# Kernel optimization log

Measured on AMD Instinct MI355X. Metric: run time of the kernel, lower is better.

The kernel has to match this reference:

```python
import jax, jax.numpy as jnp
import numpy as np

N, D_IN, D_ATTN = 8192, 48, 8


def setup_inputs() -> dict:
    key = jax.random.key(0)
    ks = jax.random.split(key, 9)
    s = 1.0 / np.sqrt(D_IN)
    return {
        "x": jax.random.normal(ks[0], (N, D_IN), jnp.float32),
        "Kw": jax.random.normal(ks[1], (D_IN, D_ATTN), jnp.float32) * s,
        "Kb": jax.random.normal(ks[2], (D_ATTN,), jnp.float32) * s,
        "Qw": jax.random.normal(ks[3], (D_IN, D_ATTN), jnp.float32) * s,
        "Qb": jax.random.normal(ks[4], (D_ATTN,), jnp.float32) * s,
        "Vw": jax.random.normal(ks[5], (D_IN, D_ATTN), jnp.float32) * s,
        "Vb": jax.random.normal(ks[6], (D_ATTN,), jnp.float32) * s,
        "Zw": jax.random.normal(ks[7], (D_ATTN, D_IN), jnp.float32) * (1.0 / np.sqrt(D_ATTN)),
        "Zb": jax.random.normal(ks[8], (D_IN,), jnp.float32) * (1.0 / np.sqrt(D_ATTN)),
    }


def reference(x, Kw, Kb, Qw, Qb, Vw, Vb, Zw, Zb):
    # Tiny QKV projections: [N,48] -> [N,8]
    Xk = x @ Kw + Kb
    Xq = x @ Qw + Qb
    Xv = x @ Vw + Vb
    # Attention over the batch/row dimension: [N,8]@[8,N] -> [N,N]
    scale = jnp.sqrt(jnp.asarray(D_ATTN, jnp.float32))
    AM = jax.nn.softmax(Xk @ Xq.T / scale, axis=1)  # torch F.softmax 2D default dim=1
    Z = AM @ Xv                                      # [N,8]
    return x + (Z @ Zw + Zb)                         # residual + output proj [N,48]
```

## Files before the change

### kernel.cpp

```cpp
#include <hip/hip_runtime.h>
#include <hip/hip_fp16.h>


#define QV_OFF   32768
#define BMAX_OFF 98304
#define PART_OFF 98560

typedef _Float16 hv2 __attribute__((ext_vector_type(2)));
union HVU { unsigned u; hv2 v; };

static __device__ __forceinline__ unsigned pku(float a, float b) {
    auto t = __builtin_amdgcn_cvt_pkrtz(a, b);
    union { decltype(t) x; unsigned u; } c; c.x = t; return c.u;
}
static __device__ __forceinline__ hv2 asV(unsigned u) { HVU t; t.u = u; return t.v; }
static __device__ __forceinline__ hv2 h2fma(hv2 a, hv2 b, hv2 c) {
#if __has_builtin(__builtin_elementwise_fma)
    return __builtin_elementwise_fma(a, b, c);
#else
    union { hv2 v; __half2 h; } A, B, C, D;
    A.v = a; B.v = b; C.v = c;
    D.h = __hfma2(A.h, B.h, C.h);
    return D.v;
#endif
}
static __device__ __forceinline__ unsigned dupL(unsigned u) {
    const unsigned lo = u & 0xFFFFu; return lo | (lo << 16);
}
static __device__ __forceinline__ unsigned dupH(unsigned u) {
    const unsigned hi = u >> 16; return hi | (hi << 16);
}

__global__ __launch_bounds__(256) void proj_kernel(
    const float* __restrict__ x,
    const float* __restrict__ Kw, const float* __restrict__ Kb,
    const float* __restrict__ Qw, const float* __restrict__ Qb,
    const float* __restrict__ Vw, const float* __restrict__ Vb,
    unsigned* __restrict__ Xksf16, unsigned* __restrict__ QV,
    float* __restrict__ bmax)
{
    __shared__ float xs[32 * 49];
    __shared__ float wAll[3 * 388];
    __shared__ float bs[24];
    __shared__ float outv[32][25];
    const int tid = threadIdx.x;
    const int r0 = blockIdx.x * 32;

    for (int i = tid; i < 1536; i += 256) {
        int r = i / 48, c = i - r * 48;
        xs[r * 49 + c] = x[r0 * 48 + i];
    }
    for (int i = tid; i < 384; i += 256) {
        wAll[i]       = Kw[i];
        wAll[388 + i] = Qw[i];
        wAll[776 + i] = Vw[i];
    }
    if (tid < 8)       bs[tid] = Kb[tid];
    else if (tid < 16) bs[tid] = Qb[tid - 8];
    else if (tid < 24) bs[tid] = Vb[tid - 16];
    __syncthreads();

    const int rl = tid >> 3;
    const int g  = tid & 7;
    const int c0 = 3 * g;
    const float* xr = &xs[rl * 49];
    const float* w0 = &wAll[((c0 + 0) >> 3) * 388 + ((c0 + 0) & 7)];
    const float* w1 = &wAll[((c0 + 1) >> 3) * 388 + ((c0 + 1) & 7)];
    const float* w2 = &wAll[((c0 + 2) >> 3) * 388 + ((c0 + 2) & 7)];
    float a0 = bs[c0], a1 = bs[c0 + 1], a2 = bs[c0 + 2];
    #pragma unroll
    for (int k = 0; k < 48; k++) {
        const float xv = xr[k];
        a0 = fmaf(xv, w0[k * 8], a0);
        a1 = fmaf(xv, w1[k * 8], a1);
        a2 = fmaf(xv, w2[k * 8], a2);
    }
    outv[rl][c0] = a0; outv[rl][c0 + 1] = a1; outv[rl][c0 + 2] = a2;
    __syncthreads();

    {
        const int p = tid >> 4;
        const int c = (tid >> 1) & 7;
        const int m = tid & 1;
        const int col = (m ? 16 : 8) + c;
        QV[(blockIdx.x * 16 + p) * 16 + m * 8 + c] =
            pku(outv[2 * p][col], outv[2 * p + 1][col]);
    }
    const float kscale = 0.51008732149f;
    if (tid < 32) {
        uint4 o;
        o.x = pku(outv[tid][0] * kscale, outv[tid][1] * kscale);
        o.y = pku(outv[tid][2] * kscale, outv[tid][3] * kscale);
        o.z = pku(outv[tid][4] * kscale, outv[tid][5] * kscale);
        o.w = pku(outv[tid][6] * kscale, outv[tid][7] * kscale);
        ((uint4*)Xksf16)[r0 + tid] = o;
    }
    if (tid >= 192 && tid < 224) {
        const int r = tid - 192;
        float n2 = 0.f;
        #pragma unroll
        for (int c = 0; c < 8; c++) n2 = fmaf(outv[r][8 + c], outv[r][8 + c], n2);
        #pragma unroll
        for (int off = 16; off > 0; off >>= 1)
            n2 = fmaxf(n2, __shfl_xor(n2, off, 64));
        if (r == 0) bmax[blockIdx.x] = n2;
    }
}

__global__ __launch_bounds__(256) void attn_kernel(
    const unsigned* __restrict__ Xksf16, const unsigned* __restrict__ QV,
    const float* __restrict__ bmax,
    float* __restrict__ part, int ppw)
{
    __shared__ uint4 slab[1024];
    const int tid  = threadIdx.x;
    const int lane = tid & 63;
    const int wv   = tid >> 6;
    const int rgrp  = blockIdx.x & 127;
    const int chunk = blockIdx.x >> 7;
    const int row   = rgrp * 64 + lane;

    float m = fmaxf(fmaxf(bmax[lane], bmax[64 + lane]),
                    fmaxf(bmax[128 + lane], bmax[192 + lane]));
    #pragma unroll
    for (int off = 32; off > 0; off >>= 1)
        m = fmaxf(m, __shfl_xor(m, off, 64));
    const float qmax2 = m;

    const uint4 kv = ((const uint4*)Xksf16)[row];
    unsigned kd[8];
    kd[0] = dupL(kv.x); kd[1] = dupH(kv.x);
    kd[2] = dupL(kv.y); kd[3] = dupH(kv.y);
    kd[4] = dupL(kv.z); kd[5] = dupH(kv.z);
    kd[6] = dupL(kv.w); kd[7] = dupH(kv.w);
    float kn2 = 0.f;
    #pragma unroll
    for (int c = 0; c < 8; c++) {
        const float kf = (float)asV(kd[c]).x;
        kn2 = fmaf(kf, kf, kn2);
    }
    const float sinit = -sqrtf(kn2 * qmax2);
    const hv2 sinit2 = asV(pku(sinit, sinit));
    const hv2 one2   = asV(0x3C003C00u);
    hv2 l2 = asV(0u), acc[8];
    #pragma unroll
    for (int c = 0; c < 8; c++) acc[c] = asV(0u);

    const uint4* QV4 = (const uint4*)QV;
    const int nt = ppw >> 6;

    for (int t = 0; t < nt; ++t) {
        for (int i = tid; i < 1024; i += 256) {
            const int w = i >> 8;
            const int j = i & 255;
            slab[i] = QV4[(size_t)((((chunk * 4 + w) * ppw + (t << 6)) << 2) + j)];
        }
        __syncthreads();

        const uint4* sw = &slab[wv << 8];
        #pragma unroll 2
        for (int p = 0; p < 64; ++p) {
            const uint4 qp0 = sw[p * 4 + 0];
            const uint4 qp1 = sw[p * 4 + 1];
            const uint4 vp0 = sw[p * 4 + 2];
            const uint4 vp1 = sw[p * 4 + 3];
            hv2 s2 = sinit2;
            s2 = h2fma(asV(kd[0]), asV(qp0.x), s2);
            s2 = h2fma(asV(kd[1]), asV(qp0.y), s2);
            s2 = h2fma(asV(kd[2]), asV(qp0.z), s2);
            s2 = h2fma(asV(kd[3]), asV(qp0.w), s2);
            s2 = h2fma(asV(kd[4]), asV(qp1.x), s2);
            s2 = h2fma(asV(kd[5]), asV(qp1.y), s2);
            s2 = h2fma(asV(kd[6]), asV(qp1.z), s2);
            s2 = h2fma(asV(kd[7]), asV(qp1.w), s2);
            const float pa = __builtin_amdgcn_exp2f((float)s2.x);
            const float pb = __builtin_amdgcn_exp2f((float)s2.y);
            const hv2 ph = asV(pku(pa, pb));
            l2 = h2fma(ph, one2, l2);
            acc[0] = h2fma(ph, asV(vp0.x), acc[0]);
            acc[1] = h2fma(ph, asV(vp0.y), acc[1]);
            acc[2] = h2fma(ph, asV(vp0.z), acc[2]);
            acc[3] = h2fma(ph, asV(vp0.w), acc[3]);
            acc[4] = h2fma(ph, asV(vp1.x), acc[4]);
            acc[5] = h2fma(ph, asV(vp1.y), acc[5]);
            acc[6] = h2fma(ph, asV(vp1.z), acc[6]);
            acc[7] = h2fma(ph, asV(vp1.w), acc[7]);
        }
        __syncthreads();
    }

    float (*red)[64][13] = reinterpret_cast<float (*)[64][13]>(slab);
    #pragma unroll
    for (int c = 0; c < 8; c++)
        red[wv][lane][c] = (float)acc[c].x + (float)acc[c].y;
    red[wv][lane][8] = (float)l2.x + (float)l2.y;
    __syncthreads();
    for (int e = tid; e < 576; e += 256) {
        const int r = e / 9, c = e - r * 9;
        const float s = red[0][r][c] + red[1][r][c] + red[2][r][c] + red[3][r][c];
        part[((size_t)chunk * 8192 + rgrp * 64 + r) * 9 + c] = s;
    }
}

__global__ __launch_bounds__(256) void finish_kernel(
    const float* __restrict__ x,
    const float* __restrict__ Zw, const float* __restrict__ Zb,
    const float* __restrict__ part, float* __restrict__ out, int nch)
{
    __shared__ float Zs[32 * 9];
    __shared__ float zw_s[384];
    __shared__ float zb_s[48];
    const int tid = threadIdx.x;
    const int r0 = blockIdx.x * 32;

    for (int i = tid; i < 384; i += 256) zw_s[i] = Zw[i];
    if (tid < 48) zb_s[tid] = Zb[tid];

    if (tid < 32) {
        const int row = r0 + tid;
        float a[9];
        #pragma unroll
        for (int c = 0; c < 9; c++) a[c] = 0.f;
        for (int ch = 0; ch < nch; ch++) {
            const float* p = part + ((size_t)ch * 8192 + row) * 9;
            #pragma unroll
            for (int c = 0; c < 9; c++) a[c] += p[c];
        }
        const float inv = 1.0f / a[8];
        #pragma unroll
        for (int c = 0; c < 8; c++) Zs[tid * 9 + c] = a[c] * inv;
    }
    __syncthreads();

    for (int e = tid; e < 32 * 48; e += 256) {
        const int r = e / 48, c = e - r * 48;
        float o = x[r0 * 48 + e] + zb_s[c];
        #pragma unroll
        for (int k = 0; k < 8; k++) o = fmaf(Zs[r * 9 + k], zw_s[k * 48 + c], o);
        out[r0 * 48 + e] = o;
    }
}

extern "C" void kernel_launch(void* const* d_in, const int* in_sizes, int n_in,
                              void* d_out, int out_size, void* d_ws, size_t ws_size,
                              hipStream_t stream) {
    const float* x  = (const float*)d_in[0];
    const float* Kw = (const float*)d_in[1];
    const float* Kb = (const float*)d_in[2];
    const float* Qw = (const float*)d_in[3];
    const float* Qb = (const float*)d_in[4];
    const float* Vw = (const float*)d_in[5];
    const float* Vb = (const float*)d_in[6];
    const float* Zw = (const float*)d_in[7];
    const float* Zb = (const float*)d_in[8];
    float* out = (float*)d_out;

    float* ws = (float*)d_ws;
    unsigned* Xksf16 = (unsigned*)ws;
    unsigned* QV     = (unsigned*)(ws + QV_OFF);
    float* bmax      = ws + BMAX_OFF;
    float* part      = ws + PART_OFF;

    int nch = 16;
    const size_t avail = ws_size / 4;
    while (nch > 1 && (size_t)PART_OFF + (size_t)nch * 8192 * 9 > avail) nch >>= 1;
    const int ppw = 1024 / nch;

    proj_kernel<<<256, 256, 0, stream>>>(x, Kw, Kb, Qw, Qb, Vw, Vb,
                                         Xksf16, QV, bmax);
    attn_kernel<<<128 * nch, 256, 0, stream>>>(Xksf16, QV, bmax, part, ppw);
    finish_kernel<<<256, 256, 0, stream>>>(x, Zw, Zb, part, out, nch);
}
```

Measured before the change: 111.0 us.

## Register-block four query rows per thread in attention and parallelize partial reduction

Each thread now handles four rows, so every Q/V pair loaded from LDS is reused four times, and row groups shrink to 32 blocks per chunk. The key-split count doubles to 32 chunks and the per-tile slab is halved. The finish kernel now spreads the partial-sum reduction over all 256 threads instead of 32. The cost is higher register pressure from 36 packed accumulators per row group, with launch bounds set to 4, a larger LDS reduction buffer, and more partial-sum traffic.

Result: slower. 119.1 us (+7.3%).

```diff
diff --git a/kernel.cpp b/kernel.cpp
--- a/kernel.cpp
+++ b/kernel.cpp
@@ -107,18 +107,20 @@
     }
 }
 
-__global__ __launch_bounds__(256) void attn_kernel(
+__global__ __launch_bounds__(256, 4) void attn_kernel(
     const unsigned* __restrict__ Xksf16, const unsigned* __restrict__ QV,
     const float* __restrict__ bmax,
     float* __restrict__ part, int ppw)
 {
-    __shared__ uint4 slab[1024];
+    __shared__ uint4 sh4[2304];
+    uint4* slab = sh4;
+    float* redf = (float*)sh4;
+
     const int tid  = threadIdx.x;
     const int lane = tid & 63;
     const int wv   = tid >> 6;
-    const int rgrp  = blockIdx.x & 127;
-    const int chunk = blockIdx.x >> 7;
-    const int row   = rgrp * 64 + lane;
+    const int rgrp  = blockIdx.x & 31;
+    const int chunk = blockIdx.x >> 5;
 
     float m = fmaxf(fmaxf(bmax[lane], bmax[64 + lane]),
                     fmaxf(bmax[128 + lane], bmax[192 + lane]));
@@ -127,78 +129,89 @@
         m = fmaxf(m, __shfl_xor(m, off, 64));
     const float qmax2 = m;
 
-    const uint4 kv = ((const uint4*)Xksf16)[row];
-    unsigned kd[8];
-    kd[0] = dupL(kv.x); kd[1] = dupH(kv.x);
-    kd[2] = dupL(kv.y); kd[3] = dupH(kv.y);
-    kd[4] = dupL(kv.z); kd[5] = dupH(kv.z);
-    kd[6] = dupL(kv.w); kd[7] = dupH(kv.w);
-    float kn2 = 0.f;
-    #pragma unroll
-    for (int c = 0; c < 8; c++) {
-        const float kf = (float)asV(kd[c]).x;
-        kn2 = fmaf(kf, kf, kn2);
-    }
-    const float sinit = -sqrtf(kn2 * qmax2);
-    const hv2 sinit2 = asV(pku(sinit, sinit));
-    const hv2 one2   = asV(0x3C003C00u);
-    hv2 l2 = asV(0u), acc[8];
-    #pragma unroll
-    for (int c = 0; c < 8; c++) acc[c] = asV(0u);
+    unsigned kd[4][8];
+    hv2 sinit2[4], l2[4], acc[4][8];
+    const hv2 one2 = asV(0x3C003C00u);
+    #pragma unroll
+    for (int i = 0; i < 4; ++i) {
+        const uint4 kv = ((const uint4*)Xksf16)[rgrp * 256 + i * 64 + lane];
+        kd[i][0] = dupL(kv.x); kd[i][1] = dupH(kv.x);
+        kd[i][2] = dupL(kv.y); kd[i][3] = dupH(kv.y);
+        kd[i][4] = dupL(kv.z); kd[i][5] = dupH(kv.z);
+        kd[i][6] = dupL(kv.w); kd[i][7] = dupH(kv.w);
+        float kn2 = 0.f;
+        #pragma unroll
+        for (int c = 0; c < 8; c++) {
+            const float kf = (float)asV(kd[i][c]).x;
+            kn2 = fmaf(kf, kf, kn2);
+        }
+        const float sinit = -sqrtf(kn2 * qmax2);
+        sinit2[i] = asV(pku(sinit, sinit));
+        l2[i] = asV(0u);
+        #pragma unroll
+        for (int c = 0; c < 8; c++) acc[i][c] = asV(0u);
+    }
 
     const uint4* QV4 = (const uint4*)QV;
-    const int nt = ppw >> 6;
+    const int nt = ppw >> 5;
 
     for (int t = 0; t < nt; ++t) {
-        for (int i = tid; i < 1024; i += 256) {
-            const int w = i >> 8;
-            const int j = i & 255;
-            slab[i] = QV4[(size_t)((((chunk * 4 + w) * ppw + (t << 6)) << 2) + j)];
+        for (int i = tid; i < 512; i += 256) {
+            const int w = i >> 7;
+            const int j = i & 127;
+            slab[i] = QV4[(size_t)((((chunk * 4 + w) * ppw + (t << 5)) << 2) + j)];
         }
         __syncthreads();
 
-        const uint4* sw = &slab[wv << 8];
+        const uint4* sw = &slab[wv << 7];
         #pragma unroll 2
-        for (int p = 0; p < 64; ++p) {
+        for (int p = 0; p < 32; ++p) {
             const uint4 qp0 = sw[p * 4 + 0];
             const uint4 qp1 = sw[p * 4 + 1];
             const uint4 vp0 = sw[p * 4 + 2];
             const uint4 vp1 = sw[p * 4 + 3];
-            hv2 s2 = sinit2;
-            s2 = h2fma(asV(kd[0]), asV(qp0.x), s2);
-            s2 = h2fma(asV(kd[1]), asV(qp0.y), s2);
-            s2 = h2fma(asV(kd[2]), asV(qp0.z), s2);
-            s2 = h2fma(asV(kd[3]), asV(qp0.w), s2);
-            s2 = h2fma(asV(kd[4]), asV(qp1.x), s2);
-            s2 = h2fma(asV(kd[5]), asV(qp1.y), s2);
-            s2 = h2fma(asV(kd[6]), asV(qp1.z), s2);
-            s2 = h2fma(asV(kd[7]), asV(qp1.w), s2);
-            const float pa = __builtin_amdgcn_exp2f((float)s2.x);
-            const float pb = __builtin_amdgcn_exp2f((float)s2.y);
-            const hv2 ph = asV(pku(pa, pb));
-            l2 = h2fma(ph, one2, l2);
-            acc[0] = h2fma(ph, asV(vp0.x), acc[0]);
-            acc[1] = h2fma(ph, asV(vp0.y), acc[1]);
-            acc[2] = h2fma(ph, asV(vp0.z), acc[2]);
-            acc[3] = h2fma(ph, asV(vp0.w), acc[3]);
-            acc[4] = h2fma(ph, asV(vp1.x), acc[4]);
-            acc[5] = h2fma(ph, asV(vp1.y), acc[5]);
-            acc[6] = h2fma(ph, asV(vp1.z), acc[6]);
-            acc[7] = h2fma(ph, asV(vp1.w), acc[7]);
+            #pragma unroll
+            for (int i = 0; i < 4; ++i) {
+                hv2 s2 = sinit2[i];
+                s2 = h2fma(asV(kd[i][0]), asV(qp0.x), s2);
+                s2 = h2fma(asV(kd[i][1]), asV(qp0.y), s2);
+                s2 = h2fma(asV(kd[i][2]), asV(qp0.z), s2);
+                s2 = h2fma(asV(kd[i][3]), asV(qp0.w), s2);
+                s2 = h2fma(asV(kd[i][4]), asV(qp1.x), s2);
+                s2 = h2fma(asV(kd[i][5]), asV(qp1.y), s2);
+                s2 = h2fma(asV(kd[i][6]), asV(qp1.z), s2);
+                s2 = h2fma(asV(kd[i][7]), asV(qp1.w), s2);
+                const float pa = __builtin_amdgcn_exp2f((float)s2.x);
+                const float pb = __builtin_amdgcn_exp2f((float)s2.y);
+                const hv2 ph = asV(pku(pa, pb));
+                l2[i] = h2fma(ph, one2, l2[i]);
+                acc[i][0] = h2fma(ph, asV(vp0.x), acc[i][0]);
+                acc[i][1] = h2fma(ph, asV(vp0.y), acc[i][1]);
+                acc[i][2] = h2fma(ph, asV(vp0.z), acc[i][2]);
+                acc[i][3] = h2fma(ph, asV(vp0.w), acc[i][3]);
+                acc[i][4] = h2fma(ph, asV(vp1.x), acc[i][4]);
+                acc[i][5] = h2fma(ph, asV(vp1.y), acc[i][5]);
+                acc[i][6] = h2fma(ph, asV(vp1.z), acc[i][6]);
+                acc[i][7] = h2fma(ph, asV(vp1.w), acc[i][7]);
+            }
         }
         __syncthreads();
     }
 
-    float (*red)[64][13] = reinterpret_cast<float (*)[64][13]>(slab);
-    #pragma unroll
-    for (int c = 0; c < 8; c++)
-        red[wv][lane][c] = (float)acc[c].x + (float)acc[c].y;
-    red[wv][lane][8] = (float)l2.x + (float)l2.y;
-    __syncthreads();
-    for (int e = tid; e < 576; e += 256) {
+    #pragma unroll
+    for (int i = 0; i < 4; ++i) {
+        const int r = i * 64 + lane;
+        #pragma unroll
+        for (int c = 0; c < 8; c++)
+            redf[(wv * 256 + r) * 9 + c] = (float)acc[i][c].x + (float)acc[i][c].y;
+        redf[(wv * 256 + r) * 9 + 8] = (float)l2[i].x + (float)l2[i].y;
+    }
+    __syncthreads();
+    for (int e = tid; e < 2304; e += 256) {
         const int r = e / 9, c = e - r * 9;
-        const float s = red[0][r][c] + red[1][r][c] + red[2][r][c] + red[3][r][c];
-        part[((size_t)chunk * 8192 + rgrp * 64 + r) * 9 + c] = s;
+        const float s = redf[(0 * 256 + r) * 9 + c] + redf[(1 * 256 + r) * 9 + c]
+                      + redf[(2 * 256 + r) * 9 + c] + redf[(3 * 256 + r) * 9 + c];
+        part[((size_t)chunk * 8192 + rgrp * 256 + r) * 9 + c] = s;
     }
 }
 
@@ -208,6 +221,7 @@
     const float* __restrict__ part, float* __restrict__ out, int nch)
 {
     __shared__ float Zs[32 * 9];
+    __shared__ float Zl[32];
     __shared__ float zw_s[384];
     __shared__ float zb_s[48];
     const int tid = threadIdx.x;
@@ -216,19 +230,18 @@
     for (int i = tid; i < 384; i += 256) zw_s[i] = Zw[i];
     if (tid < 48) zb_s[tid] = Zb[tid];
 
-    if (tid < 32) {
-        const int row = r0 + tid;
-        float a[9];
-        #pragma unroll
-        for (int c = 0; c < 9; c++) a[c] = 0.f;
+    {
+        const int r = tid >> 3, c = tid & 7;
+        float a = 0.f, l = 0.f;
+        #pragma unroll 4
         for (int ch = 0; ch < nch; ch++) {
-            const float* p = part + ((size_t)ch * 8192 + row) * 9;
-            #pragma unroll
-            for (int c = 0; c < 9; c++) a[c] += p[c];
-        }
-        const float inv = 1.0f / a[8];
-        #pragma unroll
-        for (int c = 0; c < 8; c++) Zs[tid * 9 + c] = a[c] * inv;
+            const float* p = part + ((size_t)ch * 8192 + r0 + r) * 9;
+            a += p[c];
+            if (c == 0) l += p[8];
+        }
+        if (c == 0) Zl[r] = l;
+        __syncthreads();
+        Zs[r * 9 + c] = a * (1.0f / Zl[r]);
     }
     __syncthreads();
 
@@ -261,13 +274,13 @@
     float* bmax      = ws + BMAX_OFF;
     float* part      = ws + PART_OFF;
 
-    int nch = 16;
+    int nch = 32;
     const size_t avail = ws_size / 4;
     while (nch > 1 && (size_t)PART_OFF + (size_t)nch * 8192 * 9 > avail) nch >>= 1;
     const int ppw = 1024 / nch;
 
     proj_kernel<<<256, 256, 0, stream>>>(x, Kw, Kb, Qw, Qb, Vw, Vb,
                                          Xksf16, QV, bmax);
-    attn_kernel<<<128 * nch, 256, 0, stream>>>(Xksf16, QV, bmax, part, ppw);
+    attn_kernel<<<32 * nch, 256, 0, stream>>>(Xksf16, QV, bmax, part, ppw);
     finish_kernel<<<256, 256, 0, stream>>>(x, Zw, Zb, part, out, nch);
 }
```
